# Kernel tuning notes

Measured on AMD Instinct MI355X. Metric: run time of the kernel, lower is better.

Reference implementation:

```python
import jax, jax.numpy as jnp
import numpy as np

B, L, D, DF, E = 8, 2048, 256, 1024, 1


def _layer_norm(x, g, b):
    mu = jnp.mean(x, axis=-1, keepdims=True)
    var = jnp.mean((x - mu) ** 2, axis=-1, keepdims=True)
    return (x - mu) * jax.lax.rsqrt(var + 1e-5) * g + b


def _ema_scan(z, a):
    # diagonal linear SSM: h_t = a*h_{t-1} + (1-a)*z_t, scanned over seq axis
    def step(h, zt):
        h = a * h + (1.0 - a) * zt
        return h, h
    zT = jnp.swapaxes(z, 0, 1)  # [L,B,D]
    h0 = jnp.zeros((z.shape[0], z.shape[2]), z.dtype)
    _, hs = jax.lax.scan(step, h0, zT)
    return jnp.swapaxes(hs, 0, 1)


def _mamba_block(x, m, Win, a_logit, Wout):
    zg = (x * m) @ Win                      # [B,L,2D]
    z, g = jnp.split(zg, 2, axis=-1)
    h = _ema_scan(z, jax.nn.sigmoid(a_logit))
    return ((h * jax.nn.silu(g)) @ Wout) * m


def _graph_agg(x, m, A_list, We):
    out = jnp.zeros_like(x)
    for e in range(We.shape[0]):
        A = A_list[e]
        agg = jnp.einsum('bij,bjd->bid', A, x * m)  # neighbor aggregation
        deg = jnp.clip(jnp.sum(A, axis=-1, keepdims=True), 1.0, None)
        out = out + (agg / deg) @ We[e]
    return jax.nn.relu(out) * m


def _masked_gather(x, idx, vc):
    # emulate: x_out[b,:vc] = x[b, idx[b,:vc]]; x_out[b,vc:] = x[b,vc:]
    pos = jnp.arange(x.shape[1])[None, :]
    im = jnp.where(pos < vc, idx, pos)
    return jnp.take_along_axis(x, im[:, :, None], axis=1)


def _forward(node_embedding, adjacency, gm1_Win, gm1_a_logit, gm1_Wout, gm2_We,
             gm_Win, gm_a_logit, gm_Wout, gm_We, ln1_g, ln1_b, ln2_g, ln2_b,
             ffn_W1, ffn_b1, ffn_W2, ffn_b2, Wv, bv,
             node_mask, sorted_list, reverse_list):
    X = node_embedding
    m = node_mask[:, :, None].astype(X.dtype)
    vc = jnp.sum(node_mask, axis=1, keepdims=True)  # [B,1] valid counts
    A_list = [adjacency]
    outs = []
    for si, ri in zip(sorted_list, reverse_list):
        se = _masked_gather(X, si, vc)
        bo = _mamba_block(se, m, gm1_Win, gm1_a_logit, gm1_Wout)
        re = _masked_gather(bo, ri, vc)
        outs.append(_graph_agg(re, m, A_list, gm2_We))
    outs.append(_mamba_block(X, m, gm_Win, gm_a_logit, gm_Wout) +
                _graph_agg(X, m, A_list, gm_We))
    # stack(dim=-1) + permute(0,1,3,2) + reshape == concat along feature dim
    Y = jnp.concatenate(outs, axis=-1) @ Wv + bv
    X1 = X + _layer_norm(Y, ln1_g, ln1_b)        # AddNorm, pre_ln, eval (no dropout)
    Y2 = jax.nn.relu(X1 @ ffn_W1 + ffn_b1) @ ffn_W2 + ffn_b2
    return X1 + _layer_norm(Y2, ln2_g, ln2_b)


def setup_inputs() -> dict:
    key = jax.random.key(0)
    ks = jax.random.split(key, 20)
    X = jax.random.normal(ks[0], (B, L, D), jnp.float32)
    lengths = jax.random.randint(ks[1], (B,), L // 2, L + 1)
    pos = jnp.arange(L)[None, :]
    M = (pos < lengths[:, None]).astype(jnp.int32)
    A = (jax.random.uniform(ks[2], (B, L, L)) < 0.004).astype(jnp.float32)
    A = A * M[:, :, None].astype(jnp.float32) * M[:, None, :].astype(jnp.float32)
    inp = {'node_embedding': X, 'node_mask': M, 'adjacency': A}
    for i in range(3):
        u = jax.random.uniform(ks[3 + i], (B, L))
        u = jnp.where(pos < lengths[:, None], u, 2.0 + pos.astype(jnp.float32))
        si = jnp.argsort(u, axis=1).astype(jnp.int32)   # perm of [0,vc) in prefix
        ri = jnp.argsort(si, axis=1).astype(jnp.int32)  # inverse permutation
        inp['sorted_indices_%d' % i] = si
        inp['reverse_indices_%d' % i] = ri
    def w(k, shape):
        return 0.02 * jax.random.normal(k, shape, jnp.float32)
    inp.update(
        gm1_Win=w(ks[6], (D, 2 * D)), gm1_a_logit=w(ks[7], (D,)), gm1_Wout=w(ks[8], (D, D)),
        gm2_We=w(ks[9], (E, D, D)),
        gm_Win=w(ks[10], (D, 2 * D)), gm_a_logit=w(ks[11], (D,)), gm_Wout=w(ks[12], (D, D)),
        gm_We=w(ks[13], (E, D, D)),
        ln1_g=jnp.ones((D,), jnp.float32), ln1_b=jnp.zeros((D,), jnp.float32),
        ln2_g=jnp.ones((D,), jnp.float32), ln2_b=jnp.zeros((D,), jnp.float32),
        ffn_W1=w(ks[14], (D, DF)), ffn_b1=jnp.zeros((DF,), jnp.float32),
        ffn_W2=w(ks[15], (DF, D)), ffn_b2=jnp.zeros((D,), jnp.float32),
        Wv=w(ks[16], (4 * D, D)), bv=jnp.zeros((D,), jnp.float32),
    )
    return inp


def reference(node_embedding, node_mask, adjacency,
              sorted_indices_0, sorted_indices_1, sorted_indices_2,
              reverse_indices_0, reverse_indices_1, reverse_indices_2,
              gm1_Win, gm1_a_logit, gm1_Wout, gm2_We,
              gm_Win, gm_a_logit, gm_Wout, gm_We,
              ln1_g, ln1_b, ln2_g, ln2_b,
              ffn_W1, ffn_b1, ffn_W2, ffn_b2, Wv, bv):
    return _forward(node_embedding, adjacency, gm1_Win, gm1_a_logit, gm1_Wout, gm2_We,
                    gm_Win, gm_a_logit, gm_Wout, gm_We, ln1_g, ln1_b, ln2_g, ln2_b,
                    ffn_W1, ffn_b1, ffn_W2, ffn_b2, Wv, bv,
                    node_mask,
                    [sorted_indices_0, sorted_indices_1, sorted_indices_2],
                    [reverse_indices_0, reverse_indices_1, reverse_indices_2])
```

## Files before the change

### kernel.cpp

```cpp
#include <hip/hip_runtime.h>

typedef unsigned short u16;
typedef unsigned int u32;
typedef unsigned long long u64;

#define BB 8
#define LL 2048
#define DD 256
#define NB (BB * LL)
#define NBR 4
#define NRT (NBR * NB)
#define NCH 64
#define CHL (LL / NCH)
#define CAP 64

typedef __attribute__((ext_vector_type(8))) __bf16 bf16x8;
typedef __attribute__((ext_vector_type(4))) float f32x4;

__device__ __forceinline__ float b2f(u16 u) {
    union { u32 u; float f; } x; x.u = ((u32)u) << 16; return x.f;
}
__device__ __forceinline__ u16 f2b(float f) {
    union { float f; u32 u; } x; x.f = f;
    u32 r = (x.u >> 16) & 1u;
    x.u += 0x7FFFu + r;
    return (u16)(x.u >> 16);
}
__device__ __forceinline__ float sigm(float x) { return 1.f / (1.f + __expf(-x)); }

#define GLD(gp, lp) __builtin_amdgcn_global_load_lds( \
    (const __attribute__((address_space(1))) void*)(gp), \
    (__attribute__((address_space(3))) void*)(lp), 16, 0, 0)

struct TrArgs {
    const float* s[9];
    u16* d[9];
    int K[9], N[9], tr[9];
    int beg[11];
    const float* xsrc;
    const int* maskp;
    u16* xdst;
};
__global__ void transpose_all(TrArgs a) {
    int blk = blockIdx.x;
    int i = 0;
    while (blk >= a.beg[i + 1]) ++i;
    if (i == 9) {
        int g = (blk - a.beg[9]) * 256 + threadIdx.x;
        int r = g >> 6;
        float4 v = a.maskp[r] ? *(const float4*)(a.xsrc + (size_t)g * 4)
                              : (float4){0.f, 0.f, 0.f, 0.f};
        union { u64 q; u16 h[4]; } pk;
        pk.h[0] = f2b(v.x); pk.h[1] = f2b(v.y); pk.h[2] = f2b(v.z); pk.h[3] = f2b(v.w);
        *(u64*)(a.xdst + (size_t)g * 4) = pk.q;
        return;
    }
    int idx = (blk - a.beg[i]) * 256 + threadIdx.x;
    int K = a.K[i], N = a.N[i];
    if (idx >= K * N) return;
    if (a.tr[i]) {
        int k = idx / N, n = idx - k * N;
        a.d[i][(size_t)n * K + k] = f2b(a.s[i][idx]);
    } else {
        a.d[i][idx] = f2b(a.s[i][idx]);
    }
}

__global__ void csr_kernel(const float* __restrict__ Adj,
                           const int* __restrict__ ri0, const int* __restrict__ ri1,
                           const int* __restrict__ ri2,
                           int* __restrict__ csr4, int* __restrict__ cnt,
                           float* __restrict__ deg) {
    __shared__ int lidx[4][CAP];
    __shared__ int lcnt[4], pre[4], tot;
    int row = blockIdx.x;
    int w = threadIdx.x >> 6, lane = threadIdx.x & 63;
    int rowb = row & ~(LL - 1);
    const float* aseg = Adj + (size_t)row * LL + w * 512;
    int base = 0;
#pragma unroll
    for (int it = 0; it < 2; ++it) {
        float4 v = *(const float4*)(aseg + it * 256 + lane * 4);
#pragma unroll
        for (int e = 0; e < 4; ++e) {
            float f = (e == 0) ? v.x : (e == 1) ? v.y : (e == 2) ? v.z : v.w;
            bool nz = (f != 0.f);
            u64 m = __ballot(nz);
            if (nz) {
                int pos = base + __popcll(m & ((1ull << lane) - 1ull));
                if (pos < CAP) lidx[w][pos] = w * 512 + it * 256 + lane * 4 + e;
            }
            base += __popcll(m);
        }
    }
    if (lane == 0) lcnt[w] = base;
    __syncthreads();
    if (threadIdx.x == 0) {
        int s = 0;
#pragma unroll
        for (int i = 0; i < 4; ++i) { pre[i] = s; s += lcnt[i]; }
        tot = s;
    }
    __syncthreads();
    int cw = lcnt[w]; if (cw > CAP) cw = CAP;
    int pw = pre[w];
    for (int i = lane; i < cw; i += 64) {
        int gpos = pw + i;
        if (gpos < CAP) {
            int j = lidx[w][i];
            csr4[((size_t)(3 * NB + row)) * CAP + gpos] = j;
            csr4[((size_t)(0 * NB + row)) * CAP + gpos] = ri0[rowb + j];
            csr4[((size_t)(1 * NB + row)) * CAP + gpos] = ri1[rowb + j];
            csr4[((size_t)(2 * NB + row)) * CAP + gpos] = ri2[rowb + j];
        }
    }
    if (threadIdx.x == 0) {
        int t = tot;
        cnt[row] = t < CAP ? t : CAP;
        deg[row] = (float)(t < 1 ? 1 : t);
    }
}

__global__ __launch_bounds__(256)
void gemm_win_kernel(const u16* __restrict__ Xb,
                     const int* __restrict__ si0, const int* __restrict__ si1,
                     const int* __restrict__ si2,
                     const u16* __restrict__ Bt1, const u16* __restrict__ Bt2,
                     u16* __restrict__ zbuf, u16* __restrict__ gbuf)
{
    __shared__ __align__(16) u16 As[2][128 * 32];
    __shared__ __align__(16) u16 Bs[2][128 * 32];
    int tid = threadIdx.x, lane = tid & 63;
    int w = tid >> 6, wm = w >> 1, wn = w & 1;
    int rowBase = blockIdx.x * 128, colBase = blockIdx.y * 128;
    const u16* Bt = (rowBase < 3 * NB) ? Bt1 : Bt2;

    const u16* pa[2];
    const u16* pb[2];
#pragma unroll
    for (int rep = 0; rep < 2; ++rep) {
        int s = rep * 256 + tid;
        int row = s >> 2, kk = (s & 3) << 3;
        int rg = rowBase + row;
        int br = rg >> 14, r = rg & (NB - 1), b = r >> 11, l = r & (LL - 1);
        int src = (br == 0) ? si0[r] : (br == 1) ? si1[r] : (br == 2) ? si2[r] : l;
        pa[rep] = Xb + ((size_t)(b << 11) + src) * DD + kk;
        pb[rep] = Bt + (size_t)(colBase + row) * 256 + kk;
    }

    f32x4 acc[4][4];
#pragma unroll
    for (int m = 0; m < 4; ++m)
#pragma unroll
        for (int n = 0; n < 4; ++n) acc[m][n] = (f32x4){0.f, 0.f, 0.f, 0.f};

#pragma unroll
    for (int rep = 0; rep < 2; ++rep) {
        int s = rep * 256 + tid;
        GLD(pa[rep], As[0] + s * 8);
        GLD(pb[rep], Bs[0] + s * 8);
    }
    int p = 0;
    for (int t = 0; t < 8; ++t) {
        if (t + 1 < 8) {
            int k0 = (t + 1) * 32;
#pragma unroll
            for (int rep = 0; rep < 2; ++rep) {
                int s = rep * 256 + tid;
                GLD(pa[rep] + k0, As[p ^ 1] + s * 8);
                GLD(pb[rep] + k0, Bs[p ^ 1] + s * 8);
            }
            asm volatile("s_waitcnt vmcnt(4)" ::: "memory");
        } else {
            asm volatile("s_waitcnt vmcnt(0)" ::: "memory");
        }
        __builtin_amdgcn_s_barrier();
        int kq = (lane >> 4) << 3;
        bf16x8 av[4], bw[4];
#pragma unroll
        for (int m = 0; m < 4; ++m)
            av[m] = *(const bf16x8*)(As[p] + (wm * 64 + m * 16 + (lane & 15)) * 32 + kq);
#pragma unroll
        for (int n = 0; n < 4; ++n)
            bw[n] = *(const bf16x8*)(Bs[p] + (wn * 64 + n * 16 + (lane & 15)) * 32 + kq);
#pragma unroll
        for (int m = 0; m < 4; ++m)
#pragma unroll
            for (int n = 0; n < 4; ++n)
                acc[m][n] = __builtin_amdgcn_mfma_f32_16x16x32_bf16(av[m], bw[n], acc[m][n], 0, 0, 0);
        __builtin_amdgcn_s_barrier();
        p ^= 1;
    }

    u16* Cz;
    int cb;
    if (colBase < 256) { Cz = zbuf; cb = colBase; }
    else               { Cz = gbuf; cb = colBase - 256; }
    int cBase = cb + wn * 64 + (lane & 15);
    int rBase = rowBase + wm * 64 + ((lane >> 4) << 2);
#pragma unroll
    for (int m = 0; m < 4; ++m)
#pragma unroll
        for (int n = 0; n < 4; ++n)
#pragma unroll
            for (int r = 0; r < 4; ++r)
                Cz[(size_t)(rBase + m * 16 + r) * 256 + (cBase + n * 16)] = f2b(acc[m][n][r]);
}

__global__ __launch_bounds__(256)
void gemm_kernel(const u16* __restrict__ A1, const u16* __restrict__ A2, int asplit,
                 const u16* __restrict__ Bt1, const u16* __restrict__ Bt2,
                 const u16* __restrict__ Bt3, int split1, int split2,
                 void* __restrict__ Cout, const float* __restrict__ bias,
                 int N, int K, int mode)
{
    __shared__ __align__(16) u16 As[2][128 * 32];
    __shared__ __align__(16) u16 Bs[2][128 * 32];
    int tid = threadIdx.x;
    int lane = tid & 63;
    int w = tid >> 6, wm = w >> 1, wn = w & 1;
    int rowBase = blockIdx.x * 128, colBase = blockIdx.y * 128;
    const u16* Bt = (rowBase < split1) ? Bt1 : (rowBase < split2) ? Bt2 : Bt3;
    const u16* Arow = (rowBase < asplit) ? A1 + (size_t)rowBase * K
                                         : A2 + (size_t)(rowBase - asplit) * K;

    const u16* pa[2];
    const u16* pb[2];
#pragma unroll
    for (int rep = 0; rep < 2; ++rep) {
        int s = rep * 256 + tid;
        int row = s >> 2, kk = (s & 3) << 3;
        pa[rep] = Arow + (size_t)row * K + kk;
        pb[rep] = Bt + (size_t)(colBase + row) * K + kk;
    }

    f32x4 acc[4][4];
#pragma unroll
    for (int m = 0; m < 4; ++m)
#pragma unroll
        for (int n = 0; n < 4; ++n) acc[m][n] = (f32x4){0.f, 0.f, 0.f, 0.f};

    int nt = K >> 5;
#pragma unroll
    for (int rep = 0; rep < 2; ++rep) {
        int s = rep * 256 + tid;
        GLD(pa[rep], As[0] + s * 8);
        GLD(pb[rep], Bs[0] + s * 8);
    }
    int p = 0;
    for (int t = 0; t < nt; ++t) {
        if (t + 1 < nt) {
            int k0 = (t + 1) << 5;
#pragma unroll
            for (int rep = 0; rep < 2; ++rep) {
                int s = rep * 256 + tid;
                GLD(pa[rep] + k0, As[p ^ 1] + s * 8);
                GLD(pb[rep] + k0, Bs[p ^ 1] + s * 8);
            }
            asm volatile("s_waitcnt vmcnt(4)" ::: "memory");
        } else {
            asm volatile("s_waitcnt vmcnt(0)" ::: "memory");
        }
        __builtin_amdgcn_s_barrier();
        int kq = (lane >> 4) << 3;
        bf16x8 av[4], bw[4];
#pragma unroll
        for (int m = 0; m < 4; ++m)
            av[m] = *(const bf16x8*)(As[p] + (wm * 64 + m * 16 + (lane & 15)) * 32 + kq);
#pragma unroll
        for (int n = 0; n < 4; ++n)
            bw[n] = *(const bf16x8*)(Bs[p] + (wn * 64 + n * 16 + (lane & 15)) * 32 + kq);
#pragma unroll
        for (int m = 0; m < 4; ++m)
#pragma unroll
            for (int n = 0; n < 4; ++n)
                acc[m][n] = __builtin_amdgcn_mfma_f32_16x16x32_bf16(av[m], bw[n], acc[m][n], 0, 0, 0);
        __builtin_amdgcn_s_barrier();
        p ^= 1;
    }

    int cBase = colBase + wn * 64 + (lane & 15);
    int rBase = rowBase + wm * 64 + ((lane >> 4) << 2);
    u16* C = (u16*)Cout;
    float bz[4];
#pragma unroll
    for (int n = 0; n < 4; ++n) bz[n] = bias ? bias[cBase + n * 16] : 0.f;
#pragma unroll
    for (int m = 0; m < 4; ++m)
#pragma unroll
        for (int n = 0; n < 4; ++n)
#pragma unroll
            for (int r = 0; r < 4; ++r) {
                float v = acc[m][n][r] + bz[n];
                if (mode == 1) v = v > 0.f ? v : 0.f;
                C[(size_t)(rBase + m * 16 + r) * N + (cBase + n * 16)] = f2b(v);
            }
}

__global__ __launch_bounds__(256)
void gemm_splitk2_kernel(const u16* __restrict__ A, const u16* __restrict__ Bt,
                         u16* __restrict__ C0, u16* __restrict__ C1)
{
    __shared__ __align__(16) u16 As[2][128 * 32];
    __shared__ __align__(16) u16 Bs[2][128 * 32];
    int tid = threadIdx.x;
    int lane = tid & 63;
    int w = tid >> 6, wm = w >> 1, wn = w & 1;
    int rowBase = blockIdx.x * 128, colBase = blockIdx.y * 128;
    int koff = blockIdx.z * 512;

    const u16* pa[2];
    const u16* pb[2];
#pragma unroll
    for (int rep = 0; rep < 2; ++rep) {
        int s = rep * 256 + tid;
        int row = s >> 2, kk = (s & 3) << 3;
        pa[rep] = A + (size_t)(rowBase + row) * 1024 + koff + kk;
        pb[rep] = Bt + (size_t)(colBase + row) * 1024 + koff + kk;
    }

    f32x4 acc[4][4];
#pragma unroll
    for (int m = 0; m < 4; ++m)
#pragma unroll
        for (int n = 0; n < 4; ++n) acc[m][n] = (f32x4){0.f, 0.f, 0.f, 0.f};

#pragma unroll
    for (int rep = 0; rep < 2; ++rep) {
        int s = rep * 256 + tid;
        GLD(pa[rep], As[0] + s * 8);
        GLD(pb[rep], Bs[0] + s * 8);
    }
    int p = 0;
    for (int t = 0; t < 16; ++t) {
        if (t + 1 < 16) {
            int k0 = (t + 1) << 5;
#pragma unroll
            for (int rep = 0; rep < 2; ++rep) {
                int s = rep * 256 + tid;
                GLD(pa[rep] + k0, As[p ^ 1] + s * 8);
                GLD(pb[rep] + k0, Bs[p ^ 1] + s * 8);
            }
            asm volatile("s_waitcnt vmcnt(4)" ::: "memory");
        } else {
            asm volatile("s_waitcnt vmcnt(0)" ::: "memory");
        }
        __builtin_amdgcn_s_barrier();
        int kq = (lane >> 4) << 3;
        bf16x8 av[4], bw[4];
#pragma unroll
        for (int m = 0; m < 4; ++m)
            av[m] = *(const bf16x8*)(As[p] + (wm * 64 + m * 16 + (lane & 15)) * 32 + kq);
#pragma unroll
        for (int n = 0; n < 4; ++n)
            bw[n] = *(const bf16x8*)(Bs[p] + (wn * 64 + n * 16 + (lane & 15)) * 32 + kq);
#pragma unroll
        for (int m = 0; m < 4; ++m)
#pragma unroll
            for (int n = 0; n < 4; ++n)
                acc[m][n] = __builtin_amdgcn_mfma_f32_16x16x32_bf16(av[m], bw[n], acc[m][n], 0, 0, 0);
        __builtin_amdgcn_s_barrier();
        p ^= 1;
    }

    u16* C = blockIdx.z ? C1 : C0;
    int cBase = colBase + wn * 64 + (lane & 15);
    int rBase = rowBase + wm * 64 + ((lane >> 4) << 2);
#pragma unroll
    for (int m = 0; m < 4; ++m)
#pragma unroll
        for (int n = 0; n < 4; ++n)
#pragma unroll
            for (int r = 0; r < 4; ++r)
                C[(size_t)(rBase + m * 16 + r) * 256 + (cBase + n * 16)] = f2b(acc[m][n][r]);
}

__global__ void scan_carry_kernel(const u16* __restrict__ z4, const float* __restrict__ alog1,
                                  const float* __restrict__ alog2, float* __restrict__ carry) {
    int bid = blockIdx.x;
    int br = bid >> 9, b = (bid >> 6) & 7, c = bid & 63;
    int d0 = threadIdx.x * 2;
    const float* al = (br < 3) ? alog1 : alog2;
    float aA = sigm(al[d0]), aB = sigm(al[d0 + 1]);
    float hA = 0.f, hB = 0.f;
    const u16* zp = z4 + ((size_t)(br * NB + b * LL + c * CHL) * DD) + d0;
    for (int t = 0; t < CHL; ++t) {
        u32 v = *(const u32*)(zp + (size_t)t * DD);
        hA = aA * hA + (1.f - aA) * b2f((u16)v);
        hB = aB * hB + (1.f - aB) * b2f((u16)(v >> 16));
    }
    carry[(size_t)bid * DD + d0] = hA;
    carry[(size_t)bid * DD + d0 + 1] = hB;
}

__global__ void scan_apply_kernel(const u16* __restrict__ z4, const u16* __restrict__ g4,
                                  const float* __restrict__ alog1, const float* __restrict__ alog2,
                                  const float* __restrict__ carry, u16* __restrict__ U4) {
    int bid = blockIdx.x;
    int br = bid >> 9, b = (bid >> 6) & 7, c = bid & 63;
    int d0 = threadIdx.x * 2;
    const float* al = (br < 3) ? alog1 : alog2;
    float aA = sigm(al[d0]), aB = sigm(al[d0 + 1]);
    float aPA = aA, aPB = aB;
#pragma unroll
    for (int i = 0; i < 5; ++i) { aPA *= aPA; aPB *= aPB; }
    float hA = 0.f, hB = 0.f;
    const float* cp = carry + ((size_t)((br * 8 + b) * NCH)) * DD + d0;
    for (int cc = 0; cc < c; ++cc) {
        float2 cv = *(const float2*)(cp + (size_t)cc * DD);
        hA = cv.x + aPA * hA;
        hB = cv.y + aPB * hB;
    }
    size_t rowOff = ((size_t)(br * NB + b * LL + c * CHL)) * DD + d0;
    const u16* zp = z4 + rowOff;
    const u16* gp = g4 + rowOff;
    u16* up = U4 + rowOff;
    for (int t = 0; t < CHL; ++t) {
        u32 zv = *(const u32*)(zp + (size_t)t * DD);
        u32 gv = *(const u32*)(gp + (size_t)t * DD);
        float gA = b2f((u16)gv), gB = b2f((u16)(gv >> 16));
        hA = aA * hA + (1.f - aA) * b2f((u16)zv);
        hB = aB * hB + (1.f - aB) * b2f((u16)(zv >> 16));
        u32 o = (u32)f2b(hA * gA * sigm(gA)) | ((u32)f2b(hB * gB * sigm(gB)) << 16);
        *(u32*)(up + (size_t)t * DD) = o;
    }
}

__global__ void agg4_kernel(const u16* __restrict__ V5, const int* __restrict__ csr4,
                            const int* __restrict__ cnt, const float* __restrict__ deg,
                            const int* __restrict__ maskp, u16* __restrict__ Yin) {
    int tr = threadIdx.x & 31;
    int rsub = threadIdx.x >> 5;
    int rg = blockIdx.x * 8 + rsub;
    int br = rg >> 14, r = rg & (NB - 1), b = r >> 11;
    int n = cnt[r];
    const int* lst = csr4 + ((size_t)(br * NB + r)) * CAP;
    const u16* srcB = V5 + ((size_t)((br < 3 ? br : 4) * NB + (b << 11))) * DD + tr * 8;
    float acc[8] = {0.f, 0.f, 0.f, 0.f, 0.f, 0.f, 0.f, 0.f};
    int i = 0;
    for (; i + 4 <= n; i += 4) {
        int4 il = *(const int4*)(lst + i);
        union { uint4 q; u16 h[8]; } v0, v1, v2, v3;
        v0.q = *(const uint4*)(srcB + (size_t)il.x * DD);
        v1.q = *(const uint4*)(srcB + (size_t)il.y * DD);
        v2.q = *(const uint4*)(srcB + (size_t)il.z * DD);
        v3.q = *(const uint4*)(srcB + (size_t)il.w * DD);
#pragma unroll
        for (int k = 0; k < 8; ++k)
            acc[k] += b2f(v0.h[k]) + b2f(v1.h[k]) + b2f(v2.h[k]) + b2f(v3.h[k]);
    }
    for (; i < n; ++i) {
        int idx = lst[i];
        union { uint4 q; u16 h[8]; } v;
        v.q = *(const uint4*)(srcB + (size_t)idx * DD);
#pragma unroll
        for (int k = 0; k < 8; ++k) acc[k] += b2f(v.h[k]);
    }
    float inv = 1.f / deg[r];
    int msk = maskp[r];
    union { uint4 q; u16 h[8]; } mo;
    if (br == 3) mo.q = *(const uint4*)(V5 + ((size_t)(3 * NB + r)) * DD + tr * 8);
    union { uint4 q; u16 h[8]; } o;
#pragma unroll
    for (int k = 0; k < 8; ++k) {
        float v = acc[k] * inv;
        v = v > 0.f ? v : 0.f;
        if (br == 3) v += b2f(mo.h[k]);
        v = msk ? v : 0.f;
        o.h[k] = f2b(v);
    }
    *(uint4*)(Yin + (size_t)r * 1024 + (br << 8) + tr * 8) = o.q;
}

__global__ void ln1_kernel(const u16* __restrict__ Ya, const u16* __restrict__ Yb,
                           const float* __restrict__ bvp,
                           const float* __restrict__ X, const float* __restrict__ gp,
                           const float* __restrict__ bp, u16* __restrict__ X1b) {
    int wv = threadIdx.x >> 6, lane = threadIdx.x & 63;
    int r = blockIdx.x * 4 + wv;
    int d0 = lane << 2;
    union { u64 q; u16 h[4]; } ya, yb;
    ya.q = *(const u64*)(Ya + (size_t)r * DD + d0);
    yb.q = *(const u64*)(Yb + (size_t)r * DD + d0);
    float4 bb = *(const float4*)(bvp + d0);
    float x[4];
#pragma unroll
    for (int k = 0; k < 4; ++k) x[k] = b2f(ya.h[k]) + b2f(yb.h[k]) + (&bb.x)[k];
    float s = x[0] + x[1] + x[2] + x[3];
#pragma unroll
    for (int o = 32; o > 0; o >>= 1) s += __shfl_xor(s, o, 64);
    float mu = s * (1.f / DD);
    float dx[4], ss = 0.f;
#pragma unroll
    for (int k = 0; k < 4; ++k) { dx[k] = x[k] - mu; ss += dx[k] * dx[k]; }
#pragma unroll
    for (int o = 32; o > 0; o >>= 1) ss += __shfl_xor(ss, o, 64);
    float rstd = rsqrtf(ss * (1.f / DD) + 1e-5f);
    float4 g4 = *(const float4*)(gp + d0);
    float4 b4 = *(const float4*)(bp + d0);
    float4 xv = *(const float4*)(X + (size_t)r * DD + d0);
    union { u64 q; u16 h[4]; } pk;
#pragma unroll
    for (int k = 0; k < 4; ++k) {
        float y = dx[k] * rstd * (&g4.x)[k] + (&b4.x)[k];
        pk.h[k] = f2b((&xv.x)[k] + y);
    }
    *(u64*)(X1b + (size_t)r * DD + d0) = pk.q;
}

__global__ void ln2_kernel(const u16* __restrict__ Ya, const u16* __restrict__ Yb,
                           const float* __restrict__ b2p,
                           const u16* __restrict__ X1b, const float* __restrict__ gp,
                           const float* __restrict__ bp, float* __restrict__ Out) {
    int wv = threadIdx.x >> 6, lane = threadIdx.x & 63;
    int r = blockIdx.x * 4 + wv;
    int d0 = lane << 2;
    union { u64 q; u16 h[4]; } ya, yb, x1;
    ya.q = *(const u64*)(Ya + (size_t)r * DD + d0);
    yb.q = *(const u64*)(Yb + (size_t)r * DD + d0);
    x1.q = *(const u64*)(X1b + (size_t)r * DD + d0);
    float4 bb = *(const float4*)(b2p + d0);
    float x[4];
#pragma unroll
    for (int k = 0; k < 4; ++k) x[k] = b2f(ya.h[k]) + b2f(yb.h[k]) + (&bb.x)[k];
    float s = x[0] + x[1] + x[2] + x[3];
#pragma unroll
    for (int o = 32; o > 0; o >>= 1) s += __shfl_xor(s, o, 64);
    float mu = s * (1.f / DD);
    float dx[4], ss = 0.f;
#pragma unroll
    for (int k = 0; k < 4; ++k) { dx[k] = x[k] - mu; ss += dx[k] * dx[k]; }
#pragma unroll
    for (int o = 32; o > 0; o >>= 1) ss += __shfl_xor(ss, o, 64);
    float rstd = rsqrtf(ss * (1.f / DD) + 1e-5f);
    float4 g4 = *(const float4*)(gp + d0);
    float4 b4 = *(const float4*)(bp + d0);
    float o4[4];
#pragma unroll
    for (int k = 0; k < 4; ++k)
        o4[k] = b2f(x1.h[k]) + dx[k] * rstd * (&g4.x)[k] + (&b4.x)[k];
    *(float4*)(Out + (size_t)r * DD + d0) = (float4){o4[0], o4[1], o4[2], o4[3]};
}

extern "C" void kernel_launch(void* const* d_in, const int* in_sizes, int n_in,
                              void* d_out, int out_size, void* d_ws, size_t ws_size,
                              hipStream_t stream) {
    const float* X      = (const float*)d_in[0];
    const int* maskp    = (const int*)d_in[1];
    const float* Adj    = (const float*)d_in[2];
    const int* si[3]    = { (const int*)d_in[3], (const int*)d_in[5], (const int*)d_in[7] };
    const int* ri[3]    = { (const int*)d_in[4], (const int*)d_in[6], (const int*)d_in[8] };
    const float* gm1_Win  = (const float*)d_in[9];
    const float* gm1_alog = (const float*)d_in[10];
    const float* gm1_Wout = (const float*)d_in[11];
    const float* gm2_We   = (const float*)d_in[12];
    const float* gm_Win   = (const float*)d_in[13];
    const float* gm_alog  = (const float*)d_in[14];
    const float* gm_Wout  = (const float*)d_in[15];
    const float* gm_We    = (const float*)d_in[16];
    const float* ln1_g    = (const float*)d_in[17];
    const float* ln1_b    = (const float*)d_in[18];
    const float* ln2_g    = (const float*)d_in[19];
    const float* ln2_b    = (const float*)d_in[20];
    const float* ffn_W1   = (const float*)d_in[21];
    const float* ffn_b1   = (const float*)d_in[22];
    const float* ffn_W2   = (const float*)d_in[23];
    const float* ffn_b2   = (const float*)d_in[24];
    const float* Wv       = (const float*)d_in[25];
    const float* bv       = (const float*)d_in[26];
    float* Out = (float*)d_out;

    char* ws = (char*)d_ws;
    size_t off = 0;
    auto alloc = [&](size_t bytes) { size_t o = off; off += (bytes + 255) & ~(size_t)255; return o; };

    u16* WinT1  = (u16*)(ws + alloc((size_t)512 * 256 * 2));
    u16* WinT   = (u16*)(ws + alloc((size_t)512 * 256 * 2));
    u16* WoutT  = (u16*)(ws + alloc((size_t)256 * 256 * 2));
    u16* WeT1   = (u16*)(ws + alloc((size_t)256 * 256 * 2));
    u16* WeT    = (u16*)(ws + alloc((size_t)256 * 256 * 2));
    u16* WvT    = (u16*)(ws + alloc((size_t)256 * 1024 * 2));
    u16* W1T    = (u16*)(ws + alloc((size_t)1024 * 256 * 2));
    u16* W2T    = (u16*)(ws + alloc((size_t)256 * 1024 * 2));
    u16* WoutL  = (u16*)(ws + alloc((size_t)256 * 256 * 2));
    u16* Wc1T   = (u16*)(ws + alloc((size_t)256 * 256 * 2));
    u16* Xb     = (u16*)(ws + alloc((size_t)NB * DD * 2));
    int* csr4 = (int*)(ws + alloc((size_t)4 * NB * CAP * 4));
    int* cnt = (int*)(ws + alloc((size_t)NB * 4));
    float* deg = (float*)(ws + alloc((size_t)NB * 4));
    float* carry = (float*)(ws + alloc((size_t)NBR * BB * NCH * DD * 4));
    u16* zbuf = (u16*)(ws + alloc((size_t)NRT * DD * 2));
    u16* gbuf = (u16*)(ws + alloc((size_t)NRT * DD * 2));
    u16* U4   = (u16*)(ws + alloc((size_t)4 * NB * DD * 2));
    u16* V5   = (u16*)(ws + alloc((size_t)5 * NB * DD * 2));
    u16* Yin  = (u16*)(ws + alloc((size_t)NB * 1024 * 2));
    u16* tmpYa  = (u16*)(ws + alloc((size_t)NB * DD * 2));
    u16* tmpYb  = (u16*)(ws + alloc((size_t)NB * DD * 2));
    u16* X1b    = (u16*)(ws + alloc((size_t)NB * DD * 2));
    u16* H      = (u16*)(ws + alloc((size_t)NB * 1024 * 2));
    u16* tmpY2a = (u16*)(ws + alloc((size_t)NB * DD * 2));
    u16* tmpY2b = (u16*)(ws + alloc((size_t)NB * DD * 2));
    (void)ws_size; (void)in_sizes; (void)n_in; (void)out_size;

    TrArgs ta;
    const float* srcs[9] = { gm1_Win, gm_Win, gm_Wout, gm2_We, gm_We, Wv, ffn_W1, ffn_W2, gm1_Wout };
    u16* dsts[9]         = { WinT1,   WinT,   WoutT,   WeT1,   WeT,   WvT, W1T,   W2T,    WoutL };
    int Ks[9] = { 256, 256, 256, 256, 256, 1024, 256, 1024, 256 };
    int Ns[9] = { 512, 512, 256, 256, 256, 256, 1024, 256, 256 };
    int trs[9] = { 1, 1, 1, 1, 1, 1, 1, 1, 0 };
    int cum = 0;
    for (int i = 0; i < 9; ++i) {
        ta.s[i] = srcs[i]; ta.d[i] = dsts[i]; ta.K[i] = Ks[i]; ta.N[i] = Ns[i]; ta.tr[i] = trs[i];
        ta.beg[i] = cum; cum += (Ks[i] * Ns[i]) / 256;
    }
    ta.beg[9] = cum; cum += NB * DD / 4 / 256;
    ta.beg[10] = cum;
    ta.xsrc = X; ta.maskp = maskp; ta.xdst = Xb;
    transpose_all<<<cum, 256, 0, stream>>>(ta);

    csr_kernel<<<NB, 256, 0, stream>>>(Adj, ri[0], ri[1], ri[2], csr4, cnt, deg);

    gemm_kernel<<<dim3(2, 2), 256, 0, stream>>>(
        WeT1, WeT1, 1 << 30, WoutL, WoutL, WoutL, 1 << 30, 1 << 30,
        (void*)Wc1T, nullptr, 256, 256, 2);

    gemm_win_kernel<<<dim3(NRT / 128, 512 / 128), 256, 0, stream>>>(
        Xb, si[0], si[1], si[2], WinT1, WinT, zbuf, gbuf);

    scan_carry_kernel<<<NBR * BB * NCH, 128, 0, stream>>>(zbuf, gm1_alog, gm_alog, carry);
    scan_apply_kernel<<<NBR * BB * NCH, 128, 0, stream>>>(zbuf, gbuf, gm1_alog, gm_alog, carry, U4);

    gemm_kernel<<<dim3(5 * NB / 128, 2), 256, 0, stream>>>(
        U4, Xb, 4 * NB, Wc1T, WoutT, WeT, 3 * NB, 4 * NB,
        (void*)V5, nullptr, 256, 256, 2);

    agg4_kernel<<<NRT / 8, 256, 0, stream>>>(V5, csr4, cnt, deg, maskp, Yin);

    gemm_splitk2_kernel<<<dim3(NB / 128, 2, 2), 256, 0, stream>>>(Yin, WvT, tmpYa, tmpYb);

    ln1_kernel<<<NB / 4, 256, 0, stream>>>(tmpYa, tmpYb, bv, X, ln1_g, ln1_b, X1b);

    gemm_kernel<<<dim3(NB / 128, 8), 256, 0, stream>>>(
        X1b, X1b, 1 << 30, W1T, W1T, W1T, 1 << 30, 1 << 30,
        (void*)H, ffn_b1, 1024, 256, 1);

    gemm_splitk2_kernel<<<dim3(NB / 128, 2, 2), 256, 0, stream>>>(H, W2T, tmpY2a, tmpY2b);

    ln2_kernel<<<NB / 4, 256, 0, stream>>>(tmpY2a, tmpY2b, ffn_b2, X1b, ln2_g, ln2_b, Out);
}
```

Before: 253.3 us.

## Compute Win projection once per row and gather rows inside scan kernels

```diff
diff --git a/kernel.cpp b/kernel.cpp
--- a/kernel.cpp
+++ b/kernel.cpp
@@ -32,19 +32,73 @@
     (const __attribute__((address_space(1))) void*)(gp), \
     (__attribute__((address_space(3))) void*)(lp), 16, 0, 0)
 
-struct TrArgs {
+struct PrologArgs {
     const float* s[9];
     u16* d[9];
     int K[9], N[9], tr[9];
-    int beg[11];
+    int beg[12];
     const float* xsrc;
     const int* maskp;
     u16* xdst;
+    const float* Adj;
+    const int* ri0; const int* ri1; const int* ri2;
+    int* csr4; int* cnt; float* deg;
 };
-__global__ void transpose_all(TrArgs a) {
+__global__ void prolog_kernel(PrologArgs a) {
     int blk = blockIdx.x;
     int i = 0;
     while (blk >= a.beg[i + 1]) ++i;
+    if (i == 10) {
+        __shared__ int lidx[4][CAP];
+        __shared__ int lcnt[4], pre[4], tot;
+        int row = blk - a.beg[10];
+        int w = threadIdx.x >> 6, lane = threadIdx.x & 63;
+        int rowb = row & ~(LL - 1);
+        const float* aseg = a.Adj + (size_t)row * LL + w * 512;
+        int base = 0;
+#pragma unroll
+        for (int it = 0; it < 2; ++it) {
+            float4 v = *(const float4*)(aseg + it * 256 + lane * 4);
+#pragma unroll
+            for (int e = 0; e < 4; ++e) {
+                float f = (e == 0) ? v.x : (e == 1) ? v.y : (e == 2) ? v.z : v.w;
+                bool nz = (f != 0.f);
+                u64 m = __ballot(nz);
+                if (nz) {
+                    int pos = base + __popcll(m & ((1ull << lane) - 1ull));
+                    if (pos < CAP) lidx[w][pos] = w * 512 + it * 256 + lane * 4 + e;
+                }
+                base += __popcll(m);
+            }
+        }
+        if (lane == 0) lcnt[w] = base;
+        __syncthreads();
+        if (threadIdx.x == 0) {
+            int s = 0;
+#pragma unroll
+            for (int k = 0; k < 4; ++k) { pre[k] = s; s += lcnt[k]; }
+            tot = s;
+        }
+        __syncthreads();
+        int cw = lcnt[w]; if (cw > CAP) cw = CAP;
+        int pw = pre[w];
+        for (int k = lane; k < cw; k += 64) {
+            int gpos = pw + k;
+            if (gpos < CAP) {
+                int j = lidx[w][k];
+                a.csr4[((size_t)(3 * NB + row)) * CAP + gpos] = j;
+                a.csr4[((size_t)(0 * NB + row)) * CAP + gpos] = a.ri0[rowb + j];
+                a.csr4[((size_t)(1 * NB + row)) * CAP + gpos] = a.ri1[rowb + j];
+                a.csr4[((size_t)(2 * NB + row)) * CAP + gpos] = a.ri2[rowb + j];
+            }
+        }
+        if (threadIdx.x == 0) {
+            int t = tot;
+            a.cnt[row] = t < CAP ? t : CAP;
+            a.deg[row] = (float)(t < 1 ? 1 : t);
+        }
+        return;
+    }
     if (i == 9) {
         int g = (blk - a.beg[9]) * 256 + threadIdx.x;
         int r = g >> 6;
@@ -66,74 +120,18 @@
     }
 }
 
-__global__ void csr_kernel(const float* __restrict__ Adj,
-                           const int* __restrict__ ri0, const int* __restrict__ ri1,
-                           const int* __restrict__ ri2,
-                           int* __restrict__ csr4, int* __restrict__ cnt,
-                           float* __restrict__ deg) {
-    __shared__ int lidx[4][CAP];
-    __shared__ int lcnt[4], pre[4], tot;
-    int row = blockIdx.x;
-    int w = threadIdx.x >> 6, lane = threadIdx.x & 63;
-    int rowb = row & ~(LL - 1);
-    const float* aseg = Adj + (size_t)row * LL + w * 512;
-    int base = 0;
-#pragma unroll
-    for (int it = 0; it < 2; ++it) {
-        float4 v = *(const float4*)(aseg + it * 256 + lane * 4);
-#pragma unroll
-        for (int e = 0; e < 4; ++e) {
-            float f = (e == 0) ? v.x : (e == 1) ? v.y : (e == 2) ? v.z : v.w;
-            bool nz = (f != 0.f);
-            u64 m = __ballot(nz);
-            if (nz) {
-                int pos = base + __popcll(m & ((1ull << lane) - 1ull));
-                if (pos < CAP) lidx[w][pos] = w * 512 + it * 256 + lane * 4 + e;
-            }
-            base += __popcll(m);
-        }
-    }
-    if (lane == 0) lcnt[w] = base;
-    __syncthreads();
-    if (threadIdx.x == 0) {
-        int s = 0;
-#pragma unroll
-        for (int i = 0; i < 4; ++i) { pre[i] = s; s += lcnt[i]; }
-        tot = s;
-    }
-    __syncthreads();
-    int cw = lcnt[w]; if (cw > CAP) cw = CAP;
-    int pw = pre[w];
-    for (int i = lane; i < cw; i += 64) {
-        int gpos = pw + i;
-        if (gpos < CAP) {
-            int j = lidx[w][i];
-            csr4[((size_t)(3 * NB + row)) * CAP + gpos] = j;
-            csr4[((size_t)(0 * NB + row)) * CAP + gpos] = ri0[rowb + j];
-            csr4[((size_t)(1 * NB + row)) * CAP + gpos] = ri1[rowb + j];
-            csr4[((size_t)(2 * NB + row)) * CAP + gpos] = ri2[rowb + j];
-        }
-    }
-    if (threadIdx.x == 0) {
-        int t = tot;
-        cnt[row] = t < CAP ? t : CAP;
-        deg[row] = (float)(t < 1 ? 1 : t);
-    }
-}
-
 __global__ __launch_bounds__(256)
 void gemm_win_kernel(const u16* __restrict__ Xb,
-                     const int* __restrict__ si0, const int* __restrict__ si1,
-                     const int* __restrict__ si2,
                      const u16* __restrict__ Bt1, const u16* __restrict__ Bt2,
-                     u16* __restrict__ zbuf, u16* __restrict__ gbuf)
+                     u16* __restrict__ Zz, u16* __restrict__ Zg)
 {
     __shared__ __align__(16) u16 As[2][128 * 32];
     __shared__ __align__(16) u16 Bs[2][128 * 32];
     int tid = threadIdx.x, lane = tid & 63;
     int w = tid >> 6, wm = w >> 1, wn = w & 1;
     int rowBase = blockIdx.x * 128, colBase = blockIdx.y * 128;
-    const u16* Bt = (rowBase < 3 * NB) ? Bt1 : Bt2;
+    const u16* Bt = (rowBase < NB) ? Bt1 : Bt2;
+    int arow = rowBase & (NB - 1);
 
     const u16* pa[2];
     const u16* pb[2];
@@ -141,10 +139,7 @@
     for (int rep = 0; rep < 2; ++rep) {
         int s = rep * 256 + tid;
         int row = s >> 2, kk = (s & 3) << 3;
-        int rg = rowBase + row;
-        int br = rg >> 14, r = rg & (NB - 1), b = r >> 11, l = r & (LL - 1);
-        int src = (br == 0) ? si0[r] : (br == 1) ? si1[r] : (br == 2) ? si2[r] : l;
-        pa[rep] = Xb + ((size_t)(b << 11) + src) * DD + kk;
+        pa[rep] = Xb + (size_t)(arow + row) * 256 + kk;
         pb[rep] = Bt + (size_t)(colBase + row) * 256 + kk;
     }
 
@@ -194,8 +189,8 @@
 
     u16* Cz;
     int cb;
-    if (colBase < 256) { Cz = zbuf; cb = colBase; }
-    else               { Cz = gbuf; cb = colBase - 256; }
+    if (colBase < 256) { Cz = Zz; cb = colBase; }
+    else               { Cz = Zg; cb = colBase - 256; }
     int cBase = cb + wn * 64 + (lane & 15);
     int rBase = rowBase + wm * 64 + ((lane >> 4) << 2);
 #pragma unroll
@@ -375,31 +370,52 @@
                 C[(size_t)(rBase + m * 16 + r) * 256 + (cBase + n * 16)] = f2b(acc[m][n][r]);
 }
 
-__global__ void scan_carry_kernel(const u16* __restrict__ z4, const float* __restrict__ alog1,
-                                  const float* __restrict__ alog2, float* __restrict__ carry) {
+__global__ void scan_carry_kernel(const u16* __restrict__ Zz,
+                                  const int* __restrict__ si0, const int* __restrict__ si1,
+                                  const int* __restrict__ si2,
+                                  const float* __restrict__ alog1, const float* __restrict__ alog2,
+                                  float* __restrict__ carry) {
     int bid = blockIdx.x;
     int br = bid >> 9, b = (bid >> 6) & 7, c = bid & 63;
     int d0 = threadIdx.x * 2;
     const float* al = (br < 3) ? alog1 : alog2;
+    const int* sip = (br == 0) ? si0 : (br == 1) ? si1 : (br == 2) ? si2 : nullptr;
     float aA = sigm(al[d0]), aB = sigm(al[d0 + 1]);
     float hA = 0.f, hB = 0.f;
-    const u16* zp = z4 + ((size_t)(br * NB + b * LL + c * CHL) * DD) + d0;
-    for (int t = 0; t < CHL; ++t) {
-        u32 v = *(const u32*)(zp + (size_t)t * DD);
-        hA = aA * hA + (1.f - aA) * b2f((u16)v);
-        hB = aB * hB + (1.f - aB) * b2f((u16)(v >> 16));
+    const u16* zb = Zz + (((size_t)(br < 3 ? 0 : NB) + ((size_t)b << 11)) * DD) + d0;
+    int tbase = b * LL + c * CHL;
+    for (int t0 = 0; t0 < CHL; t0 += 4) {
+        int r0, r1, r2, r3;
+        if (sip) {
+            int4 il = *(const int4*)(sip + tbase + t0);
+            r0 = il.x; r1 = il.y; r2 = il.z; r3 = il.w;
+        } else {
+            int l0 = c * CHL + t0;
+            r0 = l0; r1 = l0 + 1; r2 = l0 + 2; r3 = l0 + 3;
+        }
+        u32 v0 = *(const u32*)(zb + (size_t)r0 * DD);
+        u32 v1 = *(const u32*)(zb + (size_t)r1 * DD);
+        u32 v2 = *(const u32*)(zb + (size_t)r2 * DD);
+        u32 v3 = *(const u32*)(zb + (size_t)r3 * DD);
+        hA = aA * hA + (1.f - aA) * b2f((u16)v0); hB = aB * hB + (1.f - aB) * b2f((u16)(v0 >> 16));
+        hA = aA * hA + (1.f - aA) * b2f((u16)v1); hB = aB * hB + (1.f - aB) * b2f((u16)(v1 >> 16));
+        hA = aA * hA + (1.f - aA) * b2f((u16)v2); hB = aB * hB + (1.f - aB) * b2f((u16)(v2 >> 16));
+        hA = aA * hA + (1.f - aA) * b2f((u16)v3); hB = aB * hB + (1.f - aB) * b2f((u16)(v3 >> 16));
     }
     carry[(size_t)bid * DD + d0] = hA;
     carry[(size_t)bid * DD + d0 + 1] = hB;
 }
 
-__global__ void scan_apply_kernel(const u16* __restrict__ z4, const u16* __restrict__ g4,
+__global__ void scan_apply_kernel(const u16* __restrict__ Zz, const u16* __restrict__ Zg,
+                                  const int* __restrict__ si0, const int* __restrict__ si1,
+                                  const int* __restrict__ si2,
                                   const float* __restrict__ alog1, const float* __restrict__ alog2,
                                   const float* __restrict__ carry, u16* __restrict__ U4) {
     int bid = blockIdx.x;
     int br = bid >> 9, b = (bid >> 6) & 7, c = bid & 63;
     int d0 = threadIdx.x * 2;
     const float* al = (br < 3) ? alog1 : alog2;
+    const int* sip = (br == 0) ? si0 : (br == 1) ? si1 : (br == 2) ? si2 : nullptr;
     float aA = sigm(al[d0]), aB = sigm(al[d0 + 1]);
     float aPA = aA, aPB = aB;
 #pragma unroll
@@ -411,27 +427,46 @@
         hA = cv.x + aPA * hA;
         hB = cv.y + aPB * hB;
     }
-    size_t rowOff = ((size_t)(br * NB + b * LL + c * CHL)) * DD + d0;
-    const u16* zp = z4 + rowOff;
-    const u16* gp = g4 + rowOff;
-    u16* up = U4 + rowOff;
-    for (int t = 0; t < CHL; ++t) {
-        u32 zv = *(const u32*)(zp + (size_t)t * DD);
-        u32 gv = *(const u32*)(gp + (size_t)t * DD);
-        float gA = b2f((u16)gv), gB = b2f((u16)(gv >> 16));
-        hA = aA * hA + (1.f - aA) * b2f((u16)zv);
-        hB = aB * hB + (1.f - aB) * b2f((u16)(zv >> 16));
-        u32 o = (u32)f2b(hA * gA * sigm(gA)) | ((u32)f2b(hB * gB * sigm(gB)) << 16);
-        *(u32*)(up + (size_t)t * DD) = o;
+    size_t base = ((size_t)(br < 3 ? 0 : NB) + ((size_t)b << 11)) * DD + d0;
+    const u16* zb = Zz + base;
+    const u16* gb = Zg + base;
+    u16* up = U4 + ((size_t)(br * NB + b * LL + c * CHL)) * DD + d0;
+    int tbase = b * LL + c * CHL;
+    for (int t0 = 0; t0 < CHL; t0 += 4) {
+        int r[4];
+        if (sip) {
+            int4 il = *(const int4*)(sip + tbase + t0);
+            r[0] = il.x; r[1] = il.y; r[2] = il.z; r[3] = il.w;
+        } else {
+            int l0 = c * CHL + t0;
+            r[0] = l0; r[1] = l0 + 1; r[2] = l0 + 2; r[3] = l0 + 3;
+        }
+        u32 zv[4], gv[4];
+#pragma unroll
+        for (int e = 0; e < 4; ++e) {
+            zv[e] = *(const u32*)(zb + (size_t)r[e] * DD);
+            gv[e] = *(const u32*)(gb + (size_t)r[e] * DD);
+        }
+#pragma unroll
+        for (int e = 0; e < 4; ++e) {
+            float gA = b2f((u16)gv[e]), gB = b2f((u16)(gv[e] >> 16));
+            hA = aA * hA + (1.f - aA) * b2f((u16)zv[e]);
+            hB = aB * hB + (1.f - aB) * b2f((u16)(zv[e] >> 16));
+            u32 o = (u32)f2b(hA * gA * sigm(gA)) | ((u32)f2b(hB * gB * sigm(gB)) << 16);
+            *(u32*)(up + (size_t)(t0 + e) * DD) = o;
+        }
     }
 }
 
 __global__ void agg4_kernel(const u16* __restrict__ V5, const int* __restrict__ csr4,
                             const int* __restrict__ cnt, const float* __restrict__ deg,
                             const int* __restrict__ maskp, u16* __restrict__ Yin) {
+    int cpx = gridDim.x >> 3;
+    int obid = blockIdx.x;
+    int bid = (obid & 7) * cpx + (obid >> 3);
     int tr = threadIdx.x & 31;
     int rsub = threadIdx.x >> 5;
-    int rg = blockIdx.x * 8 + rsub;
+    int rg = bid * 8 + rsub;
     int br = rg >> 14, r = rg & (NB - 1), b = r >> 11;
     int n = cnt[r];
     const int* lst = csr4 + ((size_t)(br * NB + r)) * CAP;
@@ -589,11 +624,11 @@
     int* cnt = (int*)(ws + alloc((size_t)NB * 4));
     float* deg = (float*)(ws + alloc((size_t)NB * 4));
     float* carry = (float*)(ws + alloc((size_t)NBR * BB * NCH * DD * 4));
-    u16* zbuf = (u16*)(ws + alloc((size_t)NRT * DD * 2));
-    u16* gbuf = (u16*)(ws + alloc((size_t)NRT * DD * 2));
-    u16* U4   = (u16*)(ws + alloc((size_t)4 * NB * DD * 2));
-    u16* V5   = (u16*)(ws + alloc((size_t)5 * NB * DD * 2));
-    u16* Yin  = (u16*)(ws + alloc((size_t)NB * 1024 * 2));
+    u16* Zz  = (u16*)(ws + alloc((size_t)2 * NB * DD * 2));
+    u16* Zg  = (u16*)(ws + alloc((size_t)2 * NB * DD * 2));
+    u16* U4  = (u16*)(ws + alloc((size_t)4 * NB * DD * 2));
+    u16* V5  = (u16*)(ws + alloc((size_t)5 * NB * DD * 2));
+    u16* Yin = (u16*)(ws + alloc((size_t)NB * 1024 * 2));
     u16* tmpYa  = (u16*)(ws + alloc((size_t)NB * DD * 2));
     u16* tmpYb  = (u16*)(ws + alloc((size_t)NB * DD * 2));
     u16* X1b    = (u16*)(ws + alloc((size_t)NB * DD * 2));
@@ -602,7 +637,7 @@
     u16* tmpY2b = (u16*)(ws + alloc((size_t)NB * DD * 2));
     (void)ws_size; (void)in_sizes; (void)n_in; (void)out_size;
 
-    TrArgs ta;
+    PrologArgs ta;
     const float* srcs[9] = { gm1_Win, gm_Win, gm_Wout, gm2_We, gm_We, Wv, ffn_W1, ffn_W2, gm1_Wout };
     u16* dsts[9]         = { WinT1,   WinT,   WoutT,   WeT1,   WeT,   WvT, W1T,   W2T,    WoutL };
     int Ks[9] = { 256, 256, 256, 256, 256, 1024, 256, 1024, 256 };
@@ -614,21 +649,24 @@
         ta.beg[i] = cum; cum += (Ks[i] * Ns[i]) / 256;
     }
     ta.beg[9] = cum; cum += NB * DD / 4 / 256;
-    ta.beg[10] = cum;
+    ta.beg[10] = cum; cum += NB;
+    ta.beg[11] = cum;
     ta.xsrc = X; ta.maskp = maskp; ta.xdst = Xb;
-    transpose_all<<<cum, 256, 0, stream>>>(ta);
-
-    csr_kernel<<<NB, 256, 0, stream>>>(Adj, ri[0], ri[1], ri[2], csr4, cnt, deg);
+    ta.Adj = Adj; ta.ri0 = ri[0]; ta.ri1 = ri[1]; ta.ri2 = ri[2];
+    ta.csr4 = csr4; ta.cnt = cnt; ta.deg = deg;
+    prolog_kernel<<<cum, 256, 0, stream>>>(ta);
 
     gemm_kernel<<<dim3(2, 2), 256, 0, stream>>>(
         WeT1, WeT1, 1 << 30, WoutL, WoutL, WoutL, 1 << 30, 1 << 30,
         (void*)Wc1T, nullptr, 256, 256, 2);
 
-    gemm_win_kernel<<<dim3(NRT / 128, 512 / 128), 256, 0, stream>>>(
-        Xb, si[0], si[1], si[2], WinT1, WinT, zbuf, gbuf);
-
-    scan_carry_kernel<<<NBR * BB * NCH, 128, 0, stream>>>(zbuf, gm1_alog, gm_alog, carry);
-    scan_apply_kernel<<<NBR * BB * NCH, 128, 0, stream>>>(zbuf, gbuf, gm1_alog, gm_alog, carry, U4);
+    gemm_win_kernel<<<dim3(2 * NB / 128, 512 / 128), 256, 0, stream>>>(
+        Xb, WinT1, WinT, Zz, Zg);
+
+    scan_carry_kernel<<<NBR * BB * NCH, 128, 0, stream>>>(
+        Zz, si[0], si[1], si[2], gm1_alog, gm_alog, carry);
+    scan_apply_kernel<<<NBR * BB * NCH, 128, 0, stream>>>(
+        Zz, Zg, si[0], si[1], si[2], gm1_alog, gm_alog, carry, U4);
 
     gemm_kernel<<<dim3(5 * NB / 128, 2), 256, 0, stream>>>(
         U4, Xb, 4 * NB, Wc1T, WoutT, WeT, 3 * NB, 4 * NB,
```

Result: faster. 242.7 us (-4.2%).
